# Performance work log

Hardware: AMD Instinct MI355X
Metric: run time of the kernel (lower is better)

The kernel has to match this reference:

```python
import jax, jax.numpy as jnp
import numpy as np

N_NODES = 100000
N_EDGES = 1600000
FEATURE = 128
HIDDEN = 128
CLASSES = 64


def _sage_conv(x, src, dst, W_l, b_l, W_r, num_nodes):
    # mean aggregation of source-node features at destination nodes
    msgs = x[src]                                            # [E, F]
    agg = jax.ops.segment_sum(msgs, dst, num_segments=num_nodes)   # [N, F]
    cnt = jax.ops.segment_sum(jnp.ones((src.shape[0],), x.dtype), dst,
                              num_segments=num_nodes)        # [N]
    mean = agg / jnp.maximum(cnt, 1.0)[:, None]              # zero for isolated nodes
    return mean @ W_l.T + b_l + x @ W_r.T


def setup_inputs() -> dict:
    key = jax.random.key(0)
    ks = jax.random.split(key, 8)
    x = jax.random.normal(ks[0], (N_NODES, FEATURE), dtype=jnp.float32)
    edge_index = jax.random.randint(ks[1], (2, N_EDGES), 0, N_NODES, dtype=jnp.int64)
    s1 = 1.0 / np.sqrt(FEATURE)
    s2 = 1.0 / np.sqrt(HIDDEN)
    W1l = jax.random.uniform(ks[2], (HIDDEN, FEATURE), jnp.float32, -s1, s1)
    b1l = jnp.zeros((HIDDEN,), jnp.float32)
    W1r = jax.random.uniform(ks[3], (HIDDEN, FEATURE), jnp.float32, -s1, s1)
    W2l = jax.random.uniform(ks[4], (CLASSES, HIDDEN), jnp.float32, -s2, s2)
    b2l = jnp.zeros((CLASSES,), jnp.float32)
    W2r = jax.random.uniform(ks[5], (CLASSES, HIDDEN), jnp.float32, -s2, s2)
    return {"x": x, "edge_index": edge_index,
            "W1l": W1l, "b1l": b1l, "W1r": W1r,
            "W2l": W2l, "b2l": b2l, "W2r": W2r}


def reference(x, edge_index, W1l, b1l, W1r, W2l, b2l, W2r):
    src, dst = edge_index[0], edge_index[1]
    h = _sage_conv(x, src, dst, W1l, b1l, W1r, N_NODES)
    h = jax.nn.relu(h)
    # F.dropout(training=False) is identity in eval mode
    out = _sage_conv(h, src, dst, W2l, b2l, W2r, N_NODES)
    return jax.nn.log_softmax(out, axis=1)
```

## Files before the change

kernel.cpp:

```cpp
#include <hip/hip_runtime.h>

#define NF 128
#define NC 64
#define NBA 640
#define NBKT 196

typedef short short8 __attribute__((ext_vector_type(8)));
typedef unsigned short ushort;
typedef float f32x4 __attribute__((ext_vector_type(4)));
typedef float f32x2 __attribute__((ext_vector_type(2)));
typedef unsigned int uint;
typedef unsigned char uchar;

__device__ __forceinline__ ushort f2b(float x) {
  unsigned u = __builtin_bit_cast(unsigned, x);
  u += 0x7fffu + ((u >> 16) & 1u);
  return (ushort)(u >> 16);
}

__global__ __launch_bounds__(256) void prep_kernel(
    const float* __restrict__ x, ushort* __restrict__ xb,
    uchar* __restrict__ x8, int n4, int nb_cast,
    const float* __restrict__ W1l, const float* __restrict__ W1r,
    ushort* __restrict__ Wp1,
    const float* __restrict__ W2l, const float* __restrict__ W2r,
    ushort* __restrict__ Wp2l, ushort* __restrict__ Wp2r,
    const int* __restrict__ dst, int* __restrict__ cntA, int nE, int epb) {
  __shared__ int lh[NBKT];
  int b = blockIdx.x;
  if (b < nb_cast) {
    int i = b * 256 + threadIdx.x;
    if (i >= n4) return;
    float4 v = ((const float4*)x)[i];
    ushort4 o;
    o.x = f2b(v.x); o.y = f2b(v.y); o.z = f2b(v.z); o.w = f2b(v.w);
    ((ushort4*)xb)[i] = o;
    int u = __builtin_amdgcn_cvt_pk_fp8_f32(v.x, v.y, 0, false);
    u = __builtin_amdgcn_cvt_pk_fp8_f32(v.z, v.w, u, true);
    ((uint*)x8)[i] = (uint)u;
  } else if (b < nb_cast + 128) {
    int tid = (b - nb_cast) * 256 + threadIdx.x;
    int j = tid & 7;
    int lane = (tid >> 3) & 63;
    int tile = tid >> 9;
    int nt = tile & 7, kt = tile >> 3;
    int k = kt * 32 + ((lane >> 4) << 3) + j;
    int n = nt * 16 + (lane & 15);
    float v = (k < 128) ? W1l[n * 128 + k] : W1r[n * 128 + (k - 128)];
    Wp1[tid] = f2b(v);
  } else if (b < nb_cast + 192) {
    int tid0 = (b - nb_cast - 128) * 256 + threadIdx.x;
    int which = tid0 >> 13;
    int tid = tid0 & 8191;
    int j = tid & 7;
    int lane = (tid >> 3) & 63;
    int tile = tid >> 9;
    int nt = tile & 3, kt = tile >> 2;
    int k = kt * 32 + ((lane >> 4) << 3) + j;
    int n = nt * 16 + (lane & 15);
    const float* W = which ? W2r : W2l;
    ushort* Wp = which ? Wp2r : Wp2l;
    Wp[tid] = f2b(W[n * 128 + k]);
  } else {
    int blk = b - nb_cast - 192;
    const int t = threadIdx.x;
    for (int i = t; i < NBKT; i += 256) lh[i] = 0;
    __syncthreads();
    int s0 = blk * epb, s1 = min(nE, s0 + epb);
    for (int e = s0 + t; e < s1; e += 256) atomicAdd(&lh[dst[e] >> 9], 1);
    __syncthreads();
    for (int i = t; i < NBKT; i += 256)
      cntA[(size_t)i * NBA + blk] = lh[i];
  }
}

__global__ __launch_bounds__(256) void scanL1_kernel(const int* __restrict__ in,
                                                     int* __restrict__ out,
                                                     int* __restrict__ bsum, int L) {
  const int t = threadIdx.x;
  const int base = blockIdx.x * 1024 + t * 4;
  int v[4];
  int tsum = 0;
#pragma unroll
  for (int k = 0; k < 4; ++k) {
    v[k] = (base + k < L) ? in[base + k] : 0;
    tsum += v[k];
  }
  int lane = t & 63, wid = t >> 6;
  int x = tsum;
#pragma unroll
  for (int d = 1; d < 64; d <<= 1) {
    int y = __shfl_up(x, d);
    if (lane >= d) x += y;
  }
  __shared__ int wsum[4];
  if (lane == 63) wsum[wid] = x;
  __syncthreads();
  int wbase = 0;
  for (int w = 0; w < wid; ++w) wbase += wsum[w];
  int run = wbase + x - tsum;
#pragma unroll
  for (int k = 0; k < 4; ++k) {
    if (base + k < L) out[base + k] = run;
    run += v[k];
  }
  if (t == 0) bsum[blockIdx.x] = wsum[0] + wsum[1] + wsum[2] + wsum[3];
}

__global__ void scanL2_kernel(int* __restrict__ bsum, int nb) {
  int lane = threadIdx.x;
  int i0 = 2 * lane, i1 = 2 * lane + 1;
  int v0 = (i0 < nb) ? bsum[i0] : 0;
  int v1 = (i1 < nb) ? bsum[i1] : 0;
  int s = v0 + v1;
  int x = s;
#pragma unroll
  for (int d = 1; d < 64; d <<= 1) {
    int y = __shfl_up(x, d);
    if (lane >= d) x += y;
  }
  int ex = x - s;
  if (i0 < nb) bsum[i0] = ex;
  if (i1 < nb) bsum[i1] = ex + v0;
}

__global__ __launch_bounds__(256) void bscatA_kernel(const int* __restrict__ src,
                                                     const int* __restrict__ dst,
                                                     const int* __restrict__ cntS,
                                                     const int* __restrict__ bsum,
                                                     uint* __restrict__ tmp,
                                                     int nE, int epb) {
  __shared__ int base[NBKT];
  __shared__ int cur[NBKT];
  const int t = threadIdx.x;
  for (int i = t; i < NBKT; i += 256) {
    size_t idx = (size_t)i * NBA + blockIdx.x;
    base[i] = cntS[idx] + bsum[idx >> 10];
    cur[i] = 0;
  }
  __syncthreads();
  int s0 = blockIdx.x * epb, s1 = min(nE, s0 + epb);
  for (int e = s0 + t; e < s1; e += 256) {
    int d = dst[e];
    int s = src[e];
    int b = d >> 9;
    int r = atomicAdd(&cur[b], 1);
    tmp[base[b] + r] = ((uint)(d & 511) << 17) | (uint)s;
  }
}

__global__ __launch_bounds__(256) void bsortB_kernel(const uint* __restrict__ tmp,
                                                     const int* __restrict__ cntS,
                                                     const int* __restrict__ bsum,
                                                     int* __restrict__ esrc,
                                                     int* __restrict__ deg,
                                                     int* __restrict__ off,
                                                     int nN, int nE) {
  const int bkt = blockIdx.x;
  const int t = threadIdx.x;
  __shared__ int lh[512];
  __shared__ int cur[512];
  __shared__ int wsum[4];
  const size_t ia = (size_t)bkt * NBA;
  const int start = cntS[ia] + bsum[ia >> 10];
  int end;
  if (bkt + 1 < NBKT) {
    const size_t ib = (size_t)(bkt + 1) * NBA;
    end = cntS[ib] + bsum[ib >> 10];
  } else {
    end = nE;
  }
  lh[t] = 0;
  lh[t + 256] = 0;
  __syncthreads();
  for (int i = start + t; i < end; i += 256) {
    uint e = tmp[i];
    atomicAdd(&lh[e >> 17], 1);
  }
  __syncthreads();
  int v0 = lh[2 * t], v1 = lh[2 * t + 1];
  int ts = v0 + v1;
  int lane = t & 63, wid = t >> 6;
  int x = ts;
#pragma unroll
  for (int d = 1; d < 64; d <<= 1) {
    int y = __shfl_up(x, d);
    if (lane >= d) x += y;
  }
  if (lane == 63) wsum[wid] = x;
  __syncthreads();
  int wb = 0;
  for (int w = 0; w < wid; ++w) wb += wsum[w];
  int ex = wb + x - ts;
  cur[2 * t] = ex;
  cur[2 * t + 1] = ex + v0;
  int n0 = (bkt << 9) + 2 * t, n1 = n0 + 1;
  if (n0 < nN) { off[n0] = start + ex;      deg[n0] = v0; }
  if (n1 < nN) { off[n1] = start + ex + v0; deg[n1] = v1; }
  __syncthreads();
  for (int i = start + t; i < end; i += 256) {
    uint e = tmp[i];
    int r = atomicAdd(&cur[e >> 17], 1);
    esrc[start + r] = (int)(e & 0x1FFFFu);
  }
}

__global__ __launch_bounds__(256) void gather1_kernel(
    const uchar* __restrict__ x8, const int* __restrict__ esrc,
    const int* __restrict__ off, const int* __restrict__ deg,
    ushort* __restrict__ aggm, int nN) {
  const int w = (blockIdx.x * blockDim.x + threadIdx.x) >> 6;
  const int lane = threadIdx.x & 63;
  if (w >= nN) return;
  const int o = off[w];
  const int d = deg[w];
  const int g = lane >> 3;
  const int l = lane & 7;
  f32x2 acc[8] = {};
  int i = 0;
  for (; i + 16 <= d; i += 16) {
    int sA = esrc[o + i + g];
    int sB = esrc[o + i + 8 + g];
    uint4 vA = ((const uint4*)(x8 + (size_t)sA * NF))[l];
    uint4 vB = ((const uint4*)(x8 + (size_t)sB * NF))[l];
    acc[0] += __builtin_amdgcn_cvt_pk_f32_fp8(vA.x, false) +
              __builtin_amdgcn_cvt_pk_f32_fp8(vB.x, false);
    acc[1] += __builtin_amdgcn_cvt_pk_f32_fp8(vA.x, true) +
              __builtin_amdgcn_cvt_pk_f32_fp8(vB.x, true);
    acc[2] += __builtin_amdgcn_cvt_pk_f32_fp8(vA.y, false) +
              __builtin_amdgcn_cvt_pk_f32_fp8(vB.y, false);
    acc[3] += __builtin_amdgcn_cvt_pk_f32_fp8(vA.y, true) +
              __builtin_amdgcn_cvt_pk_f32_fp8(vB.y, true);
    acc[4] += __builtin_amdgcn_cvt_pk_f32_fp8(vA.z, false) +
              __builtin_amdgcn_cvt_pk_f32_fp8(vB.z, false);
    acc[5] += __builtin_amdgcn_cvt_pk_f32_fp8(vA.z, true) +
              __builtin_amdgcn_cvt_pk_f32_fp8(vB.z, true);
    acc[6] += __builtin_amdgcn_cvt_pk_f32_fp8(vA.w, false) +
              __builtin_amdgcn_cvt_pk_f32_fp8(vB.w, false);
    acc[7] += __builtin_amdgcn_cvt_pk_f32_fp8(vA.w, true) +
              __builtin_amdgcn_cvt_pk_f32_fp8(vB.w, true);
  }
  for (; i + 8 <= d; i += 8) {
    int s = esrc[o + i + g];
    uint4 v = ((const uint4*)(x8 + (size_t)s * NF))[l];
    acc[0] += __builtin_amdgcn_cvt_pk_f32_fp8(v.x, false);
    acc[1] += __builtin_amdgcn_cvt_pk_f32_fp8(v.x, true);
    acc[2] += __builtin_amdgcn_cvt_pk_f32_fp8(v.y, false);
    acc[3] += __builtin_amdgcn_cvt_pk_f32_fp8(v.y, true);
    acc[4] += __builtin_amdgcn_cvt_pk_f32_fp8(v.z, false);
    acc[5] += __builtin_amdgcn_cvt_pk_f32_fp8(v.z, true);
    acc[6] += __builtin_amdgcn_cvt_pk_f32_fp8(v.w, false);
    acc[7] += __builtin_amdgcn_cvt_pk_f32_fp8(v.w, true);
  }
  if (i + g < d) {
    int s = esrc[o + i + g];
    uint4 v = ((const uint4*)(x8 + (size_t)s * NF))[l];
    acc[0] += __builtin_amdgcn_cvt_pk_f32_fp8(v.x, false);
    acc[1] += __builtin_amdgcn_cvt_pk_f32_fp8(v.x, true);
    acc[2] += __builtin_amdgcn_cvt_pk_f32_fp8(v.y, false);
    acc[3] += __builtin_amdgcn_cvt_pk_f32_fp8(v.y, true);
    acc[4] += __builtin_amdgcn_cvt_pk_f32_fp8(v.z, false);
    acc[5] += __builtin_amdgcn_cvt_pk_f32_fp8(v.z, true);
    acc[6] += __builtin_amdgcn_cvt_pk_f32_fp8(v.w, false);
    acc[7] += __builtin_amdgcn_cvt_pk_f32_fp8(v.w, true);
  }
  float r[16];
#pragma unroll
  for (int k = 0; k < 8; ++k) { r[2 * k] = acc[k].x; r[2 * k + 1] = acc[k].y; }
#pragma unroll
  for (int k = 0; k < 16; ++k) {
    r[k] += __shfl_xor(r[k], 8);
    r[k] += __shfl_xor(r[k], 16);
    r[k] += __shfl_xor(r[k], 32);
  }
  if (g == 0) {
    float inv = 1.0f / fmaxf((float)d, 1.0f);
    uint4 o0, o1;
    o0.x = (uint)f2b(r[0] * inv)  | ((uint)f2b(r[1] * inv) << 16);
    o0.y = (uint)f2b(r[2] * inv)  | ((uint)f2b(r[3] * inv) << 16);
    o0.z = (uint)f2b(r[4] * inv)  | ((uint)f2b(r[5] * inv) << 16);
    o0.w = (uint)f2b(r[6] * inv)  | ((uint)f2b(r[7] * inv) << 16);
    o1.x = (uint)f2b(r[8] * inv)  | ((uint)f2b(r[9] * inv) << 16);
    o1.y = (uint)f2b(r[10] * inv) | ((uint)f2b(r[11] * inv) << 16);
    o1.z = (uint)f2b(r[12] * inv) | ((uint)f2b(r[13] * inv) << 16);
    o1.w = (uint)f2b(r[14] * inv) | ((uint)f2b(r[15] * inv) << 16);
    ((uint4*)(aggm + (size_t)w * NF))[2 * l] = o0;
    ((uint4*)(aggm + (size_t)w * NF))[2 * l + 1] = o1;
  }
}

__global__ __launch_bounds__(256) void gather2_kernel(
    const uchar* __restrict__ z8, const int* __restrict__ esrc,
    const int* __restrict__ off, const int* __restrict__ deg,
    float* __restrict__ aggz, int nN) {
  const int w = (blockIdx.x * blockDim.x + threadIdx.x) >> 6;
  const int lane = threadIdx.x & 63;
  if (w >= nN) return;
  const int o = off[w];
  const int d = deg[w];
  const int g = lane >> 3;
  const int l = lane & 7;
  f32x2 acc[4] = {};
  int i = 0;
  for (; i + 16 <= d; i += 16) {
    int sA = esrc[o + i + g];
    int sB = esrc[o + i + 8 + g];
    uint2 vA = ((const uint2*)(z8 + (size_t)sA * NC))[l];
    uint2 vB = ((const uint2*)(z8 + (size_t)sB * NC))[l];
    acc[0] += __builtin_amdgcn_cvt_pk_f32_fp8(vA.x, false) +
              __builtin_amdgcn_cvt_pk_f32_fp8(vB.x, false);
    acc[1] += __builtin_amdgcn_cvt_pk_f32_fp8(vA.x, true) +
              __builtin_amdgcn_cvt_pk_f32_fp8(vB.x, true);
    acc[2] += __builtin_amdgcn_cvt_pk_f32_fp8(vA.y, false) +
              __builtin_amdgcn_cvt_pk_f32_fp8(vB.y, false);
    acc[3] += __builtin_amdgcn_cvt_pk_f32_fp8(vA.y, true) +
              __builtin_amdgcn_cvt_pk_f32_fp8(vB.y, true);
  }
  for (; i + 8 <= d; i += 8) {
    int s = esrc[o + i + g];
    uint2 v = ((const uint2*)(z8 + (size_t)s * NC))[l];
    acc[0] += __builtin_amdgcn_cvt_pk_f32_fp8(v.x, false);
    acc[1] += __builtin_amdgcn_cvt_pk_f32_fp8(v.x, true);
    acc[2] += __builtin_amdgcn_cvt_pk_f32_fp8(v.y, false);
    acc[3] += __builtin_amdgcn_cvt_pk_f32_fp8(v.y, true);
  }
  if (i + g < d) {
    int s = esrc[o + i + g];
    uint2 v = ((const uint2*)(z8 + (size_t)s * NC))[l];
    acc[0] += __builtin_amdgcn_cvt_pk_f32_fp8(v.x, false);
    acc[1] += __builtin_amdgcn_cvt_pk_f32_fp8(v.x, true);
    acc[2] += __builtin_amdgcn_cvt_pk_f32_fp8(v.y, false);
    acc[3] += __builtin_amdgcn_cvt_pk_f32_fp8(v.y, true);
  }
  float r[8] = {acc[0].x, acc[0].y, acc[1].x, acc[1].y,
                acc[2].x, acc[2].y, acc[3].x, acc[3].y};
#pragma unroll
  for (int k = 0; k < 8; ++k) {
    r[k] += __shfl_xor(r[k], 8);
    r[k] += __shfl_xor(r[k], 16);
    r[k] += __shfl_xor(r[k], 32);
  }
  if (g == 0) {
    float inv = 1.0f / fmaxf((float)d, 1.0f);
    ((float4*)(aggz + (size_t)w * NC))[2 * l] =
        make_float4(r[0] * inv, r[1] * inv, r[2] * inv, r[3] * inv);
    ((float4*)(aggz + (size_t)w * NC))[2 * l + 1] =
        make_float4(r[4] * inv, r[5] * inv, r[6] * inv, r[7] * inv);
  }
}

__global__ __launch_bounds__(256) void layer12_mfma(
    const ushort* __restrict__ xb, const ushort* __restrict__ aggb,
    const ushort* __restrict__ Wp1, const float* __restrict__ b1,
    const ushort* __restrict__ Wp2l,
    ushort* __restrict__ hb, uchar* __restrict__ z8, int nN) {
  const int t = threadIdx.x;
  const int wv = t >> 6;
  const int lane = t & 63;
  const int base = blockIdx.x * 64;
  __shared__ ushort As[64][264];
  for (int i = t; i < 64 * 32; i += 256) {
    int r = i >> 5, cq = i & 31;
    int node = base + r;
    short8 v = {};
    if (node < nN) {
      const ushort* sp = (cq < 16) ? (aggb + (size_t)node * NF + cq * 8)
                                   : (xb + (size_t)node * NF + (cq - 16) * 8);
      v = *(const short8*)sp;
    }
    *(short8*)&As[r][cq * 8] = v;
  }
  __syncthreads();

  f32x4 acc[8] = {};
  const int arow = wv * 16 + (lane & 15);
  const int kq = (lane >> 4) * 8;
#pragma unroll
  for (int kt = 0; kt < 8; ++kt) {
    short8 af = *(const short8*)&As[arow][kt * 32 + kq];
#pragma unroll
    for (int nt = 0; nt < 8; ++nt) {
      short8 bf = *(const short8*)(Wp1 + ((size_t)(kt * 8 + nt) * 64 + lane) * 8);
      acc[nt] = __builtin_amdgcn_mfma_f32_16x16x32_bf16(af, bf, acc[nt], 0, 0, 0);
    }
  }
  const int quad = lane >> 4;
  const int cl = lane & 15;
#pragma unroll
  for (int nt = 0; nt < 8; ++nt) {
    float bj = b1[nt * 16 + cl];
#pragma unroll
    for (int r = 0; r < 4; ++r) {
      int node = base + wv * 16 + quad * 4 + r;
      ushort hv = f2b(fmaxf(acc[nt][r] + bj, 0.0f));
      As[wv * 16 + quad * 4 + r][nt * 16 + cl] = hv;
      if (node < nN) hb[(size_t)node * NF + nt * 16 + cl] = hv;
    }
  }

  f32x4 acc2[4] = {};
#pragma unroll
  for (int kt = 0; kt < 4; ++kt) {
    short8 af = *(const short8*)&As[arow][kt * 32 + kq];
#pragma unroll
    for (int nt = 0; nt < 4; ++nt) {
      short8 bf = *(const short8*)(Wp2l + ((size_t)(kt * 4 + nt) * 64 + lane) * 8);
      acc2[nt] = __builtin_amdgcn_mfma_f32_16x16x32_bf16(af, bf, acc2[nt], 0, 0, 0);
    }
  }
#pragma unroll
  for (int r = 0; r < 4; ++r) {
    int node = base + wv * 16 + quad * 4 + r;
    if (node < nN) {
      int u = __builtin_amdgcn_cvt_pk_fp8_f32(acc2[0][r], acc2[1][r], 0, false);
      u = __builtin_amdgcn_cvt_pk_fp8_f32(acc2[2][r], acc2[3][r], u, true);
      ((uint*)(z8 + (size_t)node * NC))[cl] = (uint)u;
    }
  }
}

__global__ __launch_bounds__(256) void layer2b_mfma(
    const ushort* __restrict__ hb, const float* __restrict__ aggz,
    const ushort* __restrict__ Wp, const float* __restrict__ b2,
    float* __restrict__ out, int nN) {
  const int t = threadIdx.x;
  const int wv = t >> 6;
  const int lane = t & 63;
  const int base = blockIdx.x * 64;
  __shared__ ushort As[64][136];
  for (int i = t; i < 64 * 16; i += 256) {
    int r = i >> 4, cq = i & 15;
    int node = base + r;
    short8 v = {};
    if (node < nN) v = *(const short8*)(hb + (size_t)node * NF + cq * 8);
    *(short8*)&As[r][cq * 8] = v;
  }
  __syncthreads();

  f32x4 acc[4] = {};
  const int arow = wv * 16 + (lane & 15);
  const int kq = (lane >> 4) * 8;
#pragma unroll
  for (int kt = 0; kt < 4; ++kt) {
    short8 af = *(const short8*)&As[arow][kt * 32 + kq];
#pragma unroll
    for (int nt = 0; nt < 4; ++nt) {
      short8 bf = *(const short8*)(Wp + ((size_t)(kt * 4 + nt) * 64 + lane) * 8);
      acc[nt] = __builtin_amdgcn_mfma_f32_16x16x32_bf16(af, bf, acc[nt], 0, 0, 0);
    }
  }
  const int quad = lane >> 4;
  const int cl = lane & 15;
  float bj[4];
#pragma unroll
  for (int nt = 0; nt < 4; ++nt) bj[nt] = b2[nt * 16 + cl];

#pragma unroll
  for (int r = 0; r < 4; ++r) {
    int node = base + wv * 16 + quad * 4 + r;
    int nvalid = (node < nN);
    float a0 = 0.f, a1 = 0.f, a2 = 0.f, a3 = 0.f;
    if (nvalid) {
      float4 av = ((const float4*)(aggz + (size_t)node * NC))[cl];
      a0 = av.x; a1 = av.y; a2 = av.z; a3 = av.w;
    }
    float v0 = acc[0][r] + bj[0] + a0;
    float v1 = acc[1][r] + bj[1] + a1;
    float v2 = acc[2][r] + bj[2] + a2;
    float v3 = acc[3][r] + bj[3] + a3;
    float mx = fmaxf(fmaxf(v0, v1), fmaxf(v2, v3));
#pragma unroll
    for (int s = 1; s < 16; s <<= 1) mx = fmaxf(mx, __shfl_xor(mx, s));
    float sm = expf(v0 - mx) + expf(v1 - mx) + expf(v2 - mx) + expf(v3 - mx);
#pragma unroll
    for (int s = 1; s < 16; s <<= 1) sm += __shfl_xor(sm, s);
    float ls = mx + logf(sm);
    if (nvalid) {
      float* op = out + (size_t)node * NC;
      op[0 * 16 + cl] = v0 - ls;
      op[1 * 16 + cl] = v1 - ls;
      op[2 * 16 + cl] = v2 - ls;
      op[3 * 16 + cl] = v3 - ls;
    }
  }
}

extern "C" void kernel_launch(void* const* d_in, const int* in_sizes, int n_in,
                              void* d_out, int out_size, void* d_ws, size_t ws_size,
                              hipStream_t stream) {
  const float* x   = (const float*)d_in[0];
  const int*   ei  = (const int*)d_in[1];
  const float* W1l = (const float*)d_in[2];
  const float* b1l = (const float*)d_in[3];
  const float* W1r = (const float*)d_in[4];
  const float* W2l = (const float*)d_in[5];
  const float* b2l = (const float*)d_in[6];
  const float* W2r = (const float*)d_in[7];
  float* out = (float*)d_out;

  const int nN = in_sizes[0] / NF;
  const int nE = in_sizes[1] / 2;
  const int* src = ei;
  const int* dst = ei + nE;

  char* p = (char*)d_ws;
  ushort* xb   = (ushort*)p; p += (size_t)nN * NF * 2;
  ushort* hb   = (ushort*)p; p += (size_t)nN * NF * 2;
  ushort* aggb = (ushort*)p; p += (size_t)nN * NF * 2;
  ushort* Wp1  = (ushort*)p; p += 256 * 128 * 2;
  ushort* Wp2l = (ushort*)p; p += 128 * 64 * 2;
  ushort* Wp2r = (ushort*)p; p += 128 * 64 * 2;
  int* cntA = (int*)p; p += (size_t)NBKT * NBA * 4;
  int* cntS = (int*)p; p += (size_t)NBKT * NBA * 4;
  int* bsum = (int*)p; p += 512;
  int* deg  = (int*)p; p += (size_t)nN * 4;
  int* off  = (int*)p; p += (size_t)nN * 4;
  int* esrc = (int*)p; p += (size_t)nE * 4;
  uint* tmp = (uint*)p; p += (size_t)nE * 4;

  uchar* x8   = (uchar*)hb;
  uchar* z8   = (uchar*)tmp;
  float* aggz = (float*)aggb;

  const int n4 = nN * NF / 4;
  const int nb_cast = (n4 + 255) / 256;
  const int epb = (nE + NBA - 1) / NBA;
  const int L = NBKT * NBA;
  const int nbL = (L + 1023) / 1024;

  prep_kernel<<<nb_cast + 192 + NBA, 256, 0, stream>>>(
      x, xb, x8, n4, nb_cast, W1l, W1r, Wp1, W2l, W2r, Wp2l, Wp2r,
      dst, cntA, nE, epb);

  scanL1_kernel<<<nbL, 256, 0, stream>>>(cntA, cntS, bsum, L);
  scanL2_kernel<<<1, 64, 0, stream>>>(bsum, nbL);
  bscatA_kernel<<<NBA, 256, 0, stream>>>(src, dst, cntS, bsum, tmp, nE, epb);
  bsortB_kernel<<<NBKT, 256, 0, stream>>>(tmp, cntS, bsum, esrc, deg, off, nN, nE);

  gather1_kernel<<<(nN + 3) / 4, 256, 0, stream>>>(x8, esrc, off, deg, aggb, nN);
  layer12_mfma<<<(nN + 63) / 64, 256, 0, stream>>>(xb, aggb, Wp1, b1l, Wp2l, hb, z8, nN);

  gather2_kernel<<<(nN + 3) / 4, 256, 0, stream>>>(z8, esrc, off, deg, aggz, nN);
  layer2b_mfma<<<(nN + 63) / 64, 256, 0, stream>>>(hb, aggz, Wp2r, b2l, out, nN);
}
```

Before: 298.4 us.

## Remap gather kernels to sub-wave node groups and fold second-level scan into consumers

The gather kernels now assign 16 lanes (layer 1) or 8 lanes (layer 2) per node instead of a full 64-lane wave. Each lane owns a fixed slice of the feature row and loops over all neighbors with 8-way unrolled independent loads, which removes the cross-lane shuffle reduction and the idle lanes on low-degree nodes. Separately, the tiny scanL2 kernel is removed and every block of bscatA and bsortB recomputes the 128-entry block-sum prefix in shared memory, saving one launch at the cost of redundant work. The narrower rows per lane issue smaller loads (8 bytes), which may reduce memory-level parallelism per node.

```diff
diff --git a/kernel.cpp b/kernel.cpp
--- a/kernel.cpp
+++ b/kernel.cpp
@@ -107,35 +107,35 @@
   if (t == 0) bsum[blockIdx.x] = wsum[0] + wsum[1] + wsum[2] + wsum[3];
 }
 
-__global__ void scanL2_kernel(int* __restrict__ bsum, int nb) {
-  int lane = threadIdx.x;
-  int i0 = 2 * lane, i1 = 2 * lane + 1;
-  int v0 = (i0 < nb) ? bsum[i0] : 0;
-  int v1 = (i1 < nb) ? bsum[i1] : 0;
-  int s = v0 + v1;
-  int x = s;
-#pragma unroll
-  for (int d = 1; d < 64; d <<= 1) {
-    int y = __shfl_up(x, d);
-    if (lane >= d) x += y;
-  }
-  int ex = x - s;
-  if (i0 < nb) bsum[i0] = ex;
-  if (i1 < nb) bsum[i1] = ex + v0;
-}
-
 __global__ __launch_bounds__(256) void bscatA_kernel(const int* __restrict__ src,
                                                      const int* __restrict__ dst,
                                                      const int* __restrict__ cntS,
                                                      const int* __restrict__ bsum,
                                                      uint* __restrict__ tmp,
-                                                     int nE, int epb) {
+                                                     int nE, int epb, int nbL) {
   __shared__ int base[NBKT];
   __shared__ int cur[NBKT];
+  __shared__ int sbs[128];
+  __shared__ int w0s;
   const int t = threadIdx.x;
+  int ex = 0;
+  if (t < 128) {
+    int v = (t < nbL) ? bsum[t] : 0;
+    int x = v;
+#pragma unroll
+    for (int d = 1; d < 64; d <<= 1) {
+      int y = __shfl_up(x, d);
+      if ((t & 63) >= d) x += y;
+    }
+    ex = x - v;
+    if (t == 63) w0s = x;
+  }
+  __syncthreads();
+  if (t < 128) sbs[t] = ex + ((t >= 64) ? w0s : 0);
+  __syncthreads();
   for (int i = t; i < NBKT; i += 256) {
     size_t idx = (size_t)i * NBA + blockIdx.x;
-    base[i] = cntS[idx] + bsum[idx >> 10];
+    base[i] = cntS[idx] + sbs[idx >> 10];
     cur[i] = 0;
   }
   __syncthreads();
@@ -155,18 +155,35 @@
                                                      int* __restrict__ esrc,
                                                      int* __restrict__ deg,
                                                      int* __restrict__ off,
-                                                     int nN, int nE) {
+                                                     int nN, int nE, int nbL) {
   const int bkt = blockIdx.x;
   const int t = threadIdx.x;
   __shared__ int lh[512];
   __shared__ int cur[512];
   __shared__ int wsum[4];
+  __shared__ int sbs[128];
+  __shared__ int w0s;
+  int ex0 = 0;
+  if (t < 128) {
+    int v = (t < nbL) ? bsum[t] : 0;
+    int x = v;
+#pragma unroll
+    for (int d = 1; d < 64; d <<= 1) {
+      int y = __shfl_up(x, d);
+      if ((t & 63) >= d) x += y;
+    }
+    ex0 = x - v;
+    if (t == 63) w0s = x;
+  }
+  __syncthreads();
+  if (t < 128) sbs[t] = ex0 + ((t >= 64) ? w0s : 0);
+  __syncthreads();
   const size_t ia = (size_t)bkt * NBA;
-  const int start = cntS[ia] + bsum[ia >> 10];
+  const int start = cntS[ia] + sbs[ia >> 10];
   int end;
   if (bkt + 1 < NBKT) {
     const size_t ib = (size_t)(bkt + 1) * NBA;
-    end = cntS[ib] + bsum[ib >> 10];
+    end = cntS[ib] + sbs[ib >> 10];
   } else {
     end = nE;
   }
@@ -209,144 +226,196 @@
     const uchar* __restrict__ x8, const int* __restrict__ esrc,
     const int* __restrict__ off, const int* __restrict__ deg,
     ushort* __restrict__ aggm, int nN) {
-  const int w = (blockIdx.x * blockDim.x + threadIdx.x) >> 6;
-  const int lane = threadIdx.x & 63;
+  const int w = (blockIdx.x * blockDim.x + threadIdx.x) >> 4;
+  const int l = threadIdx.x & 15;
   if (w >= nN) return;
   const int o = off[w];
   const int d = deg[w];
-  const int g = lane >> 3;
-  const int l = lane & 7;
-  f32x2 acc[8] = {};
+  const uint2* __restrict__ xp = (const uint2*)x8;
+  f32x2 a0 = {}, a1 = {}, a2 = {}, a3 = {};
   int i = 0;
-  for (; i + 16 <= d; i += 16) {
-    int sA = esrc[o + i + g];
-    int sB = esrc[o + i + 8 + g];
-    uint4 vA = ((const uint4*)(x8 + (size_t)sA * NF))[l];
-    uint4 vB = ((const uint4*)(x8 + (size_t)sB * NF))[l];
-    acc[0] += __builtin_amdgcn_cvt_pk_f32_fp8(vA.x, false) +
-              __builtin_amdgcn_cvt_pk_f32_fp8(vB.x, false);
-    acc[1] += __builtin_amdgcn_cvt_pk_f32_fp8(vA.x, true) +
-              __builtin_amdgcn_cvt_pk_f32_fp8(vB.x, true);
-    acc[2] += __builtin_amdgcn_cvt_pk_f32_fp8(vA.y, false) +
-              __builtin_amdgcn_cvt_pk_f32_fp8(vB.y, false);
-    acc[3] += __builtin_amdgcn_cvt_pk_f32_fp8(vA.y, true) +
-              __builtin_amdgcn_cvt_pk_f32_fp8(vB.y, true);
-    acc[4] += __builtin_amdgcn_cvt_pk_f32_fp8(vA.z, false) +
-              __builtin_amdgcn_cvt_pk_f32_fp8(vB.z, false);
-    acc[5] += __builtin_amdgcn_cvt_pk_f32_fp8(vA.z, true) +
-              __builtin_amdgcn_cvt_pk_f32_fp8(vB.z, true);
-    acc[6] += __builtin_amdgcn_cvt_pk_f32_fp8(vA.w, false) +
-              __builtin_amdgcn_cvt_pk_f32_fp8(vB.w, false);
-    acc[7] += __builtin_amdgcn_cvt_pk_f32_fp8(vA.w, true) +
-              __builtin_amdgcn_cvt_pk_f32_fp8(vB.w, true);
-  }
   for (; i + 8 <= d; i += 8) {
-    int s = esrc[o + i + g];
-    uint4 v = ((const uint4*)(x8 + (size_t)s * NF))[l];
-    acc[0] += __builtin_amdgcn_cvt_pk_f32_fp8(v.x, false);
-    acc[1] += __builtin_amdgcn_cvt_pk_f32_fp8(v.x, true);
-    acc[2] += __builtin_amdgcn_cvt_pk_f32_fp8(v.y, false);
-    acc[3] += __builtin_amdgcn_cvt_pk_f32_fp8(v.y, true);
-    acc[4] += __builtin_amdgcn_cvt_pk_f32_fp8(v.z, false);
-    acc[5] += __builtin_amdgcn_cvt_pk_f32_fp8(v.z, true);
-    acc[6] += __builtin_amdgcn_cvt_pk_f32_fp8(v.w, false);
-    acc[7] += __builtin_amdgcn_cvt_pk_f32_fp8(v.w, true);
-  }
-  if (i + g < d) {
-    int s = esrc[o + i + g];
-    uint4 v = ((const uint4*)(x8 + (size_t)s * NF))[l];
-    acc[0] += __builtin_amdgcn_cvt_pk_f32_fp8(v.x, false);
-    acc[1] += __builtin_amdgcn_cvt_pk_f32_fp8(v.x, true);
-    acc[2] += __builtin_amdgcn_cvt_pk_f32_fp8(v.y, false);
-    acc[3] += __builtin_amdgcn_cvt_pk_f32_fp8(v.y, true);
-    acc[4] += __builtin_amdgcn_cvt_pk_f32_fp8(v.z, false);
-    acc[5] += __builtin_amdgcn_cvt_pk_f32_fp8(v.z, true);
-    acc[6] += __builtin_amdgcn_cvt_pk_f32_fp8(v.w, false);
-    acc[7] += __builtin_amdgcn_cvt_pk_f32_fp8(v.w, true);
-  }
-  float r[16];
-#pragma unroll
-  for (int k = 0; k < 8; ++k) { r[2 * k] = acc[k].x; r[2 * k + 1] = acc[k].y; }
-#pragma unroll
-  for (int k = 0; k < 16; ++k) {
-    r[k] += __shfl_xor(r[k], 8);
-    r[k] += __shfl_xor(r[k], 16);
-    r[k] += __shfl_xor(r[k], 32);
-  }
-  if (g == 0) {
-    float inv = 1.0f / fmaxf((float)d, 1.0f);
-    uint4 o0, o1;
-    o0.x = (uint)f2b(r[0] * inv)  | ((uint)f2b(r[1] * inv) << 16);
-    o0.y = (uint)f2b(r[2] * inv)  | ((uint)f2b(r[3] * inv) << 16);
-    o0.z = (uint)f2b(r[4] * inv)  | ((uint)f2b(r[5] * inv) << 16);
-    o0.w = (uint)f2b(r[6] * inv)  | ((uint)f2b(r[7] * inv) << 16);
-    o1.x = (uint)f2b(r[8] * inv)  | ((uint)f2b(r[9] * inv) << 16);
-    o1.y = (uint)f2b(r[10] * inv) | ((uint)f2b(r[11] * inv) << 16);
-    o1.z = (uint)f2b(r[12] * inv) | ((uint)f2b(r[13] * inv) << 16);
-    o1.w = (uint)f2b(r[14] * inv) | ((uint)f2b(r[15] * inv) << 16);
-    ((uint4*)(aggm + (size_t)w * NF))[2 * l] = o0;
-    ((uint4*)(aggm + (size_t)w * NF))[2 * l + 1] = o1;
-  }
+    int s0 = esrc[o + i + 0], s1 = esrc[o + i + 1];
+    int s2 = esrc[o + i + 2], s3 = esrc[o + i + 3];
+    int s4 = esrc[o + i + 4], s5 = esrc[o + i + 5];
+    int s6 = esrc[o + i + 6], s7 = esrc[o + i + 7];
+    uint2 v0 = xp[(size_t)s0 * 16 + l];
+    uint2 v1 = xp[(size_t)s1 * 16 + l];
+    uint2 v2 = xp[(size_t)s2 * 16 + l];
+    uint2 v3 = xp[(size_t)s3 * 16 + l];
+    uint2 v4 = xp[(size_t)s4 * 16 + l];
+    uint2 v5 = xp[(size_t)s5 * 16 + l];
+    uint2 v6 = xp[(size_t)s6 * 16 + l];
+    uint2 v7 = xp[(size_t)s7 * 16 + l];
+    a0 += ((__builtin_amdgcn_cvt_pk_f32_fp8(v0.x, false) +
+            __builtin_amdgcn_cvt_pk_f32_fp8(v1.x, false)) +
+           (__builtin_amdgcn_cvt_pk_f32_fp8(v2.x, false) +
+            __builtin_amdgcn_cvt_pk_f32_fp8(v3.x, false))) +
+          ((__builtin_amdgcn_cvt_pk_f32_fp8(v4.x, false) +
+            __builtin_amdgcn_cvt_pk_f32_fp8(v5.x, false)) +
+           (__builtin_amdgcn_cvt_pk_f32_fp8(v6.x, false) +
+            __builtin_amdgcn_cvt_pk_f32_fp8(v7.x, false)));
+    a1 += ((__builtin_amdgcn_cvt_pk_f32_fp8(v0.x, true) +
+            __builtin_amdgcn_cvt_pk_f32_fp8(v1.x, true)) +
+           (__builtin_amdgcn_cvt_pk_f32_fp8(v2.x, true) +
+            __builtin_amdgcn_cvt_pk_f32_fp8(v3.x, true))) +
+          ((__builtin_amdgcn_cvt_pk_f32_fp8(v4.x, true) +
+            __builtin_amdgcn_cvt_pk_f32_fp8(v5.x, true)) +
+           (__builtin_amdgcn_cvt_pk_f32_fp8(v6.x, true) +
+            __builtin_amdgcn_cvt_pk_f32_fp8(v7.x, true)));
+    a2 += ((__builtin_amdgcn_cvt_pk_f32_fp8(v0.y, false) +
+            __builtin_amdgcn_cvt_pk_f32_fp8(v1.y, false)) +
+           (__builtin_amdgcn_cvt_pk_f32_fp8(v2.y, false) +
+            __builtin_amdgcn_cvt_pk_f32_fp8(v3.y, false))) +
+          ((__builtin_amdgcn_cvt_pk_f32_fp8(v4.y, false) +
+            __builtin_amdgcn_cvt_pk_f32_fp8(v5.y, false)) +
+           (__builtin_amdgcn_cvt_pk_f32_fp8(v6.y, false) +
+            __builtin_amdgcn_cvt_pk_f32_fp8(v7.y, false)));
+    a3 += ((__builtin_amdgcn_cvt_pk_f32_fp8(v0.y, true) +
+            __builtin_amdgcn_cvt_pk_f32_fp8(v1.y, true)) +
+           (__builtin_amdgcn_cvt_pk_f32_fp8(v2.y, true) +
+            __builtin_amdgcn_cvt_pk_f32_fp8(v3.y, true))) +
+          ((__builtin_amdgcn_cvt_pk_f32_fp8(v4.y, true) +
+            __builtin_amdgcn_cvt_pk_f32_fp8(v5.y, true)) +
+           (__builtin_amdgcn_cvt_pk_f32_fp8(v6.y, true) +
+            __builtin_amdgcn_cvt_pk_f32_fp8(v7.y, true)));
+  }
+  for (; i + 4 <= d; i += 4) {
+    int s0 = esrc[o + i + 0], s1 = esrc[o + i + 1];
+    int s2 = esrc[o + i + 2], s3 = esrc[o + i + 3];
+    uint2 v0 = xp[(size_t)s0 * 16 + l];
+    uint2 v1 = xp[(size_t)s1 * 16 + l];
+    uint2 v2 = xp[(size_t)s2 * 16 + l];
+    uint2 v3 = xp[(size_t)s3 * 16 + l];
+    a0 += (__builtin_amdgcn_cvt_pk_f32_fp8(v0.x, false) +
+           __builtin_amdgcn_cvt_pk_f32_fp8(v1.x, false)) +
+          (__builtin_amdgcn_cvt_pk_f32_fp8(v2.x, false) +
+           __builtin_amdgcn_cvt_pk_f32_fp8(v3.x, false));
+    a1 += (__builtin_amdgcn_cvt_pk_f32_fp8(v0.x, true) +
+           __builtin_amdgcn_cvt_pk_f32_fp8(v1.x, true)) +
+          (__builtin_amdgcn_cvt_pk_f32_fp8(v2.x, true) +
+           __builtin_amdgcn_cvt_pk_f32_fp8(v3.x, true));
+    a2 += (__builtin_amdgcn_cvt_pk_f32_fp8(v0.y, false) +
+           __builtin_amdgcn_cvt_pk_f32_fp8(v1.y, false)) +
+          (__builtin_amdgcn_cvt_pk_f32_fp8(v2.y, false) +
+           __builtin_amdgcn_cvt_pk_f32_fp8(v3.y, false));
+    a3 += (__builtin_amdgcn_cvt_pk_f32_fp8(v0.y, true) +
+           __builtin_amdgcn_cvt_pk_f32_fp8(v1.y, true)) +
+          (__builtin_amdgcn_cvt_pk_f32_fp8(v2.y, true) +
+           __builtin_amdgcn_cvt_pk_f32_fp8(v3.y, true));
+  }
+  for (; i < d; ++i) {
+    int s = esrc[o + i];
+    uint2 v = xp[(size_t)s * 16 + l];
+    a0 += __builtin_amdgcn_cvt_pk_f32_fp8(v.x, false);
+    a1 += __builtin_amdgcn_cvt_pk_f32_fp8(v.x, true);
+    a2 += __builtin_amdgcn_cvt_pk_f32_fp8(v.y, false);
+    a3 += __builtin_amdgcn_cvt_pk_f32_fp8(v.y, true);
+  }
+  float inv = 1.0f / fmaxf((float)d, 1.0f);
+  uint4 ov;
+  ov.x = (uint)f2b(a0.x * inv) | ((uint)f2b(a0.y * inv) << 16);
+  ov.y = (uint)f2b(a1.x * inv) | ((uint)f2b(a1.y * inv) << 16);
+  ov.z = (uint)f2b(a2.x * inv) | ((uint)f2b(a2.y * inv) << 16);
+  ov.w = (uint)f2b(a3.x * inv) | ((uint)f2b(a3.y * inv) << 16);
+  ((uint4*)(aggm + (size_t)w * NF))[l] = ov;
 }
 
 __global__ __launch_bounds__(256) void gather2_kernel(
     const uchar* __restrict__ z8, const int* __restrict__ esrc,
     const int* __restrict__ off, const int* __restrict__ deg,
     float* __restrict__ aggz, int nN) {
-  const int w = (blockIdx.x * blockDim.x + threadIdx.x) >> 6;
-  const int lane = threadIdx.x & 63;
+  const int w = (blockIdx.x * blockDim.x + threadIdx.x) >> 3;
+  const int l = threadIdx.x & 7;
   if (w >= nN) return;
   const int o = off[w];
   const int d = deg[w];
-  const int g = lane >> 3;
-  const int l = lane & 7;
-  f32x2 acc[4] = {};
+  const uint2* __restrict__ zp = (const uint2*)z8;
+  f32x2 a0 = {}, a1 = {}, a2 = {}, a3 = {};
   int i = 0;
-  for (; i + 16 <= d; i += 16) {
-    int sA = esrc[o + i + g];
-    int sB = esrc[o + i + 8 + g];
-    uint2 vA = ((const uint2*)(z8 + (size_t)sA * NC))[l];
-    uint2 vB = ((const uint2*)(z8 + (size_t)sB * NC))[l];
-    acc[0] += __builtin_amdgcn_cvt_pk_f32_fp8(vA.x, false) +
-              __builtin_amdgcn_cvt_pk_f32_fp8(vB.x, false);
-    acc[1] += __builtin_amdgcn_cvt_pk_f32_fp8(vA.x, true) +
-              __builtin_amdgcn_cvt_pk_f32_fp8(vB.x, true);
-    acc[2] += __builtin_amdgcn_cvt_pk_f32_fp8(vA.y, false) +
-              __builtin_amdgcn_cvt_pk_f32_fp8(vB.y, false);
-    acc[3] += __builtin_amdgcn_cvt_pk_f32_fp8(vA.y, true) +
-              __builtin_amdgcn_cvt_pk_f32_fp8(vB.y, true);
-  }
   for (; i + 8 <= d; i += 8) {
-    int s = esrc[o + i + g];
-    uint2 v = ((const uint2*)(z8 + (size_t)s * NC))[l];
-    acc[0] += __builtin_amdgcn_cvt_pk_f32_fp8(v.x, false);
-    acc[1] += __builtin_amdgcn_cvt_pk_f32_fp8(v.x, true);
-    acc[2] += __builtin_amdgcn_cvt_pk_f32_fp8(v.y, false);
-    acc[3] += __builtin_amdgcn_cvt_pk_f32_fp8(v.y, true);
-  }
-  if (i + g < d) {
-    int s = esrc[o + i + g];
-    uint2 v = ((const uint2*)(z8 + (size_t)s * NC))[l];
-    acc[0] += __builtin_amdgcn_cvt_pk_f32_fp8(v.x, false);
-    acc[1] += __builtin_amdgcn_cvt_pk_f32_fp8(v.x, true);
-    acc[2] += __builtin_amdgcn_cvt_pk_f32_fp8(v.y, false);
-    acc[3] += __builtin_amdgcn_cvt_pk_f32_fp8(v.y, true);
-  }
-  float r[8] = {acc[0].x, acc[0].y, acc[1].x, acc[1].y,
-                acc[2].x, acc[2].y, acc[3].x, acc[3].y};
-#pragma unroll
-  for (int k = 0; k < 8; ++k) {
-    r[k] += __shfl_xor(r[k], 8);
-    r[k] += __shfl_xor(r[k], 16);
-    r[k] += __shfl_xor(r[k], 32);
-  }
-  if (g == 0) {
-    float inv = 1.0f / fmaxf((float)d, 1.0f);
-    ((float4*)(aggz + (size_t)w * NC))[2 * l] =
-        make_float4(r[0] * inv, r[1] * inv, r[2] * inv, r[3] * inv);
-    ((float4*)(aggz + (size_t)w * NC))[2 * l + 1] =
-        make_float4(r[4] * inv, r[5] * inv, r[6] * inv, r[7] * inv);
-  }
+    int s0 = esrc[o + i + 0], s1 = esrc[o + i + 1];
+    int s2 = esrc[o + i + 2], s3 = esrc[o + i + 3];
+    int s4 = esrc[o + i + 4], s5 = esrc[o + i + 5];
+    int s6 = esrc[o + i + 6], s7 = esrc[o + i + 7];
+    uint2 v0 = zp[(size_t)s0 * 8 + l];
+    uint2 v1 = zp[(size_t)s1 * 8 + l];
+    uint2 v2 = zp[(size_t)s2 * 8 + l];
+    uint2 v3 = zp[(size_t)s3 * 8 + l];
+    uint2 v4 = zp[(size_t)s4 * 8 + l];
+    uint2 v5 = zp[(size_t)s5 * 8 + l];
+    uint2 v6 = zp[(size_t)s6 * 8 + l];
+    uint2 v7 = zp[(size_t)s7 * 8 + l];
+    a0 += ((__builtin_amdgcn_cvt_pk_f32_fp8(v0.x, false) +
+            __builtin_amdgcn_cvt_pk_f32_fp8(v1.x, false)) +
+           (__builtin_amdgcn_cvt_pk_f32_fp8(v2.x, false) +
+            __builtin_amdgcn_cvt_pk_f32_fp8(v3.x, false))) +
+          ((__builtin_amdgcn_cvt_pk_f32_fp8(v4.x, false) +
+            __builtin_amdgcn_cvt_pk_f32_fp8(v5.x, false)) +
+           (__builtin_amdgcn_cvt_pk_f32_fp8(v6.x, false) +
+            __builtin_amdgcn_cvt_pk_f32_fp8(v7.x, false)));
+    a1 += ((__builtin_amdgcn_cvt_pk_f32_fp8(v0.x, true) +
+            __builtin_amdgcn_cvt_pk_f32_fp8(v1.x, true)) +
+           (__builtin_amdgcn_cvt_pk_f32_fp8(v2.x, true) +
+            __builtin_amdgcn_cvt_pk_f32_fp8(v3.x, true))) +
+          ((__builtin_amdgcn_cvt_pk_f32_fp8(v4.x, true) +
+            __builtin_amdgcn_cvt_pk_f32_fp8(v5.x, true)) +
+           (__builtin_amdgcn_cvt_pk_f32_fp8(v6.x, true) +
+            __builtin_amdgcn_cvt_pk_f32_fp8(v7.x, true)));
+    a2 += ((__builtin_amdgcn_cvt_pk_f32_fp8(v0.y, false) +
+            __builtin_amdgcn_cvt_pk_f32_fp8(v1.y, false)) +
+           (__builtin_amdgcn_cvt_pk_f32_fp8(v2.y, false) +
+            __builtin_amdgcn_cvt_pk_f32_fp8(v3.y, false))) +
+          ((__builtin_amdgcn_cvt_pk_f32_fp8(v4.y, false) +
+            __builtin_amdgcn_cvt_pk_f32_fp8(v5.y, false)) +
+           (__builtin_amdgcn_cvt_pk_f32_fp8(v6.y, false) +
+            __builtin_amdgcn_cvt_pk_f32_fp8(v7.y, false)));
+    a3 += ((__builtin_amdgcn_cvt_pk_f32_fp8(v0.y, true) +
+            __builtin_amdgcn_cvt_pk_f32_fp8(v1.y, true)) +
+           (__builtin_amdgcn_cvt_pk_f32_fp8(v2.y, true) +
+            __builtin_amdgcn_cvt_pk_f32_fp8(v3.y, true))) +
+          ((__builtin_amdgcn_cvt_pk_f32_fp8(v4.y, true) +
+            __builtin_amdgcn_cvt_pk_f32_fp8(v5.y, true)) +
+           (__builtin_amdgcn_cvt_pk_f32_fp8(v6.y, true) +
+            __builtin_amdgcn_cvt_pk_f32_fp8(v7.y, true)));
+  }
+  for (; i + 4 <= d; i += 4) {
+    int s0 = esrc[o + i + 0], s1 = esrc[o + i + 1];
+    int s2 = esrc[o + i + 2], s3 = esrc[o + i + 3];
+    uint2 v0 = zp[(size_t)s0 * 8 + l];
+    uint2 v1 = zp[(size_t)s1 * 8 + l];
+    uint2 v2 = zp[(size_t)s2 * 8 + l];
+    uint2 v3 = zp[(size_t)s3 * 8 + l];
+    a0 += (__builtin_amdgcn_cvt_pk_f32_fp8(v0.x, false) +
+           __builtin_amdgcn_cvt_pk_f32_fp8(v1.x, false)) +
+          (__builtin_amdgcn_cvt_pk_f32_fp8(v2.x, false) +
+           __builtin_amdgcn_cvt_pk_f32_fp8(v3.x, false));
+    a1 += (__builtin_amdgcn_cvt_pk_f32_fp8(v0.x, true) +
+           __builtin_amdgcn_cvt_pk_f32_fp8(v1.x, true)) +
+          (__builtin_amdgcn_cvt_pk_f32_fp8(v2.x, true) +
+           __builtin_amdgcn_cvt_pk_f32_fp8(v3.x, true));
+    a2 += (__builtin_amdgcn_cvt_pk_f32_fp8(v0.y, false) +
+           __builtin_amdgcn_cvt_pk_f32_fp8(v1.y, false)) +
+          (__builtin_amdgcn_cvt_pk_f32_fp8(v2.y, false) +
+           __builtin_amdgcn_cvt_pk_f32_fp8(v3.y, false));
+    a3 += (__builtin_amdgcn_cvt_pk_f32_fp8(v0.y, true) +
+           __builtin_amdgcn_cvt_pk_f32_fp8(v1.y, true)) +
+          (__builtin_amdgcn_cvt_pk_f32_fp8(v2.y, true) +
+           __builtin_amdgcn_cvt_pk_f32_fp8(v3.y, true));
+  }
+  for (; i < d; ++i) {
+    int s = esrc[o + i];
+    uint2 v = zp[(size_t)s * 8 + l];
+    a0 += __builtin_amdgcn_cvt_pk_f32_fp8(v.x, false);
+    a1 += __builtin_amdgcn_cvt_pk_f32_fp8(v.x, true);
+    a2 += __builtin_amdgcn_cvt_pk_f32_fp8(v.y, false);
+    a3 += __builtin_amdgcn_cvt_pk_f32_fp8(v.y, true);
+  }
+  float inv = 1.0f / fmaxf((float)d, 1.0f);
+  ((float4*)(aggz + (size_t)w * NC))[2 * l] =
+      make_float4(a0.x * inv, a0.y * inv, a1.x * inv, a1.y * inv);
+  ((float4*)(aggz + (size_t)w * NC))[2 * l + 1] =
+      make_float4(a2.x * inv, a2.y * inv, a3.x * inv, a3.y * inv);
 }
 
 __global__ __launch_bounds__(256) void layer12_mfma(
@@ -533,13 +602,12 @@
       dst, cntA, nE, epb);
 
   scanL1_kernel<<<nbL, 256, 0, stream>>>(cntA, cntS, bsum, L);
-  scanL2_kernel<<<1, 64, 0, stream>>>(bsum, nbL);
-  bscatA_kernel<<<NBA, 256, 0, stream>>>(src, dst, cntS, bsum, tmp, nE, epb);
-  bsortB_kernel<<<NBKT, 256, 0, stream>>>(tmp, cntS, bsum, esrc, deg, off, nN, nE);
-
-  gather1_kernel<<<(nN + 3) / 4, 256, 0, stream>>>(x8, esrc, off, deg, aggb, nN);
+  bscatA_kernel<<<NBA, 256, 0, stream>>>(src, dst, cntS, bsum, tmp, nE, epb, nbL);
+  bsortB_kernel<<<NBKT, 256, 0, stream>>>(tmp, cntS, bsum, esrc, deg, off, nN, nE, nbL);
+
+  gather1_kernel<<<(nN * 16 + 255) / 256, 256, 0, stream>>>(x8, esrc, off, deg, aggb, nN);
   layer12_mfma<<<(nN + 63) / 64, 256, 0, stream>>>(xb, aggb, Wp1, b1l, Wp2l, hb, z8, nN);
 
-  gather2_kernel<<<(nN + 3) / 4, 256, 0, stream>>>(z8, esrc, off, deg, aggz, nN);
+  gather2_kernel<<<(nN * 8 + 255) / 256, 256, 0, stream>>>(z8, esrc, off, deg, aggz, nN);
   layer2b_mfma<<<(nN + 63) / 64, 256, 0, stream>>>(hb, aggz, Wp2r, b2l, out, nN);
 }
```

Result: faster. 265.7 us (-11.0%).
